# Kernel optimization log

Measured on AMD Instinct MI355X. Metric: run time of the kernel, lower is better.

Reference implementation:

```python
import jax, jax.numpy as jnp
import numpy as np

D = 256; H = 8; DH = D // H; FF = 1024; L = 2048; M = 1024


def _mlp(x, w0, b0, w1, b1, w2, b2):
    # 3-layer MLP, relu on all but last (matches MLP class)
    x = jax.nn.relu(x @ w0 + b0)
    x = jax.nn.relu(x @ w1 + b1)
    return x @ w2 + b2


def _ln(x, g, b, eps=1e-5):
    m = jnp.mean(x, axis=-1, keepdims=True)
    v = jnp.var(x, axis=-1, keepdims=True)
    return (x - m) * jax.lax.rsqrt(v + eps) * g + b


def setup_inputs():
    key = jax.random.key(0)
    ks = jax.random.split(key, 16)
    p = lambda i, shape: jax.random.normal(ks[i], shape, jnp.float32) * 0.02
    z = lambda *s: jnp.zeros(s, jnp.float32)
    o = lambda *s: jnp.ones(s, jnp.float32)
    # positions: ego covers [0, L), agent covers [L-M, 2L-M) -> exactly M shared positions
    return {
        'ego_q': jax.random.normal(ks[0], (1, L, D), jnp.float32),
        'agent_q': jax.random.normal(ks[1], (1, L, D), jnp.float32),
        'ego_pos': jnp.arange(L, dtype=jnp.int32),
        'agent_pos': jnp.arange(L, dtype=jnp.int32) + (L - M),
        'n_match': M,
        'fw0': p(2, (2 * D, D)), 'fb0': z(D),
        'fw1': p(3, (D, D)), 'fb1': z(D),
        'fw2': p(4, (D, D)), 'fb2': z(D),
        'wq': p(5, (D, D)), 'bq': z(D),
        'wk': p(6, (D, D)), 'bk': z(D),
        'wv': p(7, (D, D)), 'bv': z(D),
        'wo': p(8, (D, D)), 'bo': z(D),
        'g1': o(D), 'be1': z(D),
        'l1w': p(9, (D, FF)), 'l1b': z(FF),
        'l2w': p(10, (FF, D)), 'l2b': z(D),
        'g2': o(D), 'be2': z(D),
    }


def reference(ego_q, agent_q, ego_pos, agent_pos, n_match,
              fw0, fb0, fw1, fb1, fw2, fb2,
              wq, bq, wk, bk, wv, bv, wo, bo,
              g1, be1, l1w, l1b, l2w, l2b, g2, be2):
    La = agent_pos.shape[0]
    # vectorized replacement of the per-position dict/loop grouping:
    # for each ego position, find a matching agent position (positions sorted+unique)
    idx = jnp.clip(jnp.searchsorted(agent_pos, ego_pos), 0, La - 1)
    matched = (agent_pos[idx] == ego_pos)                     # (L,)
    pair = jnp.concatenate([ego_q, agent_q[:, idx, :]], axis=-1)  # (1, L, 2D)
    fused = _mlp(pair, fw0, fb0, fw1, fb1, fw2, fb2)          # (1, L, D)
    ego_out = jnp.where(matched[None, :, None], fused, ego_q)
    # agent queries whose positions are NOT in ego's set: indices [n_match, La)
    q = jnp.concatenate([ego_out, agent_q[:, n_match:, :]], axis=1)  # (1, 2L-M, D)
    kv = jnp.concatenate([ego_q, agent_q], axis=1)                   # (1, 2L, D)
    # MultiheadAttention (batch_first, eval mode -> no dropout)
    qh = (q @ wq + bq).reshape(1, -1, H, DH)
    kh = (kv @ wk + bk).reshape(1, -1, H, DH)
    vh = (kv @ wv + bv).reshape(1, -1, H, DH)
    scores = jnp.einsum('bqhd,bkhd->bhqk', qh, kh) * (1.0 / np.sqrt(DH))
    attn = jax.nn.softmax(scores, axis=-1)
    o = jnp.einsum('bhqk,bkhd->bqhd', attn, vh).reshape(1, -1, D) @ wo + bo
    x = _ln(q + o, g1, be1)
    ff = jax.nn.relu(x @ l1w + l1b) @ l2w + l2b
    return _ln(x + ff, g2, be2)
```

## Files before the change

### kernel.cpp

```cpp
#include <hip/hip_runtime.h>
#include <hip/hip_bf16.h>

typedef __hip_bfloat16 bf16;
typedef __bf16 bf16x8 __attribute__((ext_vector_type(8)));
typedef float  f32x16 __attribute__((ext_vector_type(16)));

__device__ __forceinline__ bool is_bf16_flag(const unsigned* g1w) {
    return *g1w == 0x3F803F80u;
}

__device__ __forceinline__ unsigned cvt_pk_bf16(float lo, float hi) {
    unsigned w;
    asm("v_cvt_pk_bf16_f32 %0, %1, %2" : "=v"(w) : "v"(lo), "v"(hi));
    return w;
}
__device__ __forceinline__ void permlane32_swap(unsigned& a, unsigned& b) {
    asm("v_permlane32_swap_b32 %0, %1" : "+v"(a), "+v"(b));
}

union FragU { unsigned u[4]; uint4 q; bf16x8 v; };

__device__ __forceinline__ float loadf(const void* p, size_t i, bool isb) {
    return isb ? __bfloat162float(((const bf16*)p)[i]) : ((const float*)p)[i];
}

__device__ __forceinline__ float4 load4rt(const void* p, size_t i, bool isb) {
    if (isb) {
        uint2 u = *(const uint2*)((const bf16*)p + i);
        float4 f;
        f.x = __uint_as_float(u.x << 16);
        f.y = __uint_as_float(u.x & 0xFFFF0000u);
        f.z = __uint_as_float(u.y << 16);
        f.w = __uint_as_float(u.y & 0xFFFF0000u);
        return f;
    }
    return *(const float4*)((const float*)p + i);
}

__device__ __forceinline__ void store4b(bf16* p, float4 v) {
    uint2 w;
    w.x = cvt_pk_bf16(v.x, v.y);
    w.y = cvt_pk_bf16(v.z, v.w);
    *(uint2*)p = w;
}

__device__ __forceinline__ float4 load4b(const bf16* p) {
    uint2 u = *(const uint2*)p;
    float4 f;
    f.x = __uint_as_float(u.x << 16);
    f.y = __uint_as_float(u.x & 0xFFFF0000u);
    f.z = __uint_as_float(u.y << 16);
    f.w = __uint_as_float(u.y & 0xFFFF0000u);
    return f;
}

#define NCVT 13
#define NWT 9
struct PreArgs {
    const void* csrc[NCVT];
    float*      cdst[NCVT];
    float       cscale[NCVT];
    int         cn4[NCVT];
    int         cblk_end[NCVT];
    int         cvt_blocks;
    const void* wsrc[NWT];
    bf16*       wdst[NWT];
    int         wK[NWT];
    int         wN[NWT];
    float       wscale[NWT];
    int         wblk_end[NWT];
    int         wt_blocks;
    const void* ego; const void* agent;
    const int*  epos; const int* apos;
    int         La;
    bf16*       pair;
    int*        mflag;
};

__global__ void preprocess_kernel(PreArgs a, const unsigned* __restrict__ g1w) {
    bool isb = is_bf16_flag(g1w);
    __shared__ float ld[64][65];
    __shared__ int s_idx[2];
    int b = blockIdx.x;
    int tid = threadIdx.x;
    if (b < a.cvt_blocks) {
        int t = 0;
        while (b >= a.cblk_end[t]) t++;
        int base = (t == 0) ? 0 : a.cblk_end[t - 1];
        int i = (b - base) * 256 + tid;
        if (i >= a.cn4[t]) return;
        float sc = a.cscale[t];
        float4 r = load4rt(a.csrc[t], (size_t)i * 4, isb);
        r.x *= sc; r.y *= sc; r.z *= sc; r.w *= sc;
        ((float4*)a.cdst[t])[i] = r;
    } else if (b < a.cvt_blocks + a.wt_blocks) {
        b -= a.cvt_blocks;
        int w = 0;
        while (b >= a.wblk_end[w]) w++;
        int base = (w == 0) ? 0 : a.wblk_end[w - 1];
        int tt = b - base;
        int tn = a.wN[w] >> 6;
        int kr = (tt / tn) * 64, nc = (tt % tn) * 64;
        int N = a.wN[w], K = a.wK[w];
        float sc = a.wscale[w];
        const void* src = a.wsrc[w];
#pragma unroll
        for (int i = 0; i < 16; i++) {
            int f = tid + i * 256;
            int r = f >> 6, c = f & 63;
            ld[r][c] = loadf(src, (size_t)(kr + r) * N + nc + c, isb) * sc;
        }
        __syncthreads();
        bf16* dst = a.wdst[w];
#pragma unroll
        for (int i = 0; i < 16; i++) {
            int f = tid + i * 256;
            int c = f >> 6, r = f & 63;
            dst[(size_t)(nc + c) * K + kr + r] = __float2bfloat16(ld[r][c]);
        }
    } else {
        b -= a.cvt_blocks + a.wt_blocks;
        int rb = tid >> 7;
        int row = b * 2 + rb;
        int cc = (tid & 127) * 4;
        if ((tid & 127) == 0) {
            int p = a.epos[row];
            int lo = 0, hi = a.La;
            while (lo < hi) { int mid = (lo + hi) >> 1; if (a.apos[mid] < p) lo = mid + 1; else hi = mid; }
            int idx = lo < a.La - 1 ? lo : a.La - 1;
            s_idx[rb] = idx;
            a.mflag[row] = (a.apos[idx] == p) ? 1 : 0;
        }
        __syncthreads();
        int idx = s_idx[rb];
        float4 v = (cc < 256) ? load4rt(a.ego, (size_t)row * 256 + cc, isb)
                              : load4rt(a.agent, (size_t)idx * 256 + (cc - 256), isb);
        store4b(a.pair + (size_t)row * 512 + cc, v);
    }
}

template<int RELU>
__device__ __forceinline__ void gemm_core(const bf16* __restrict__ A, const bf16* __restrict__ Bt,
                                          const float* __restrict__ bias, bf16* __restrict__ C,
                                          int K, int lda, int ldb, int ldc,
                                          int bm, int bn, bool addBias,
                                          char* sA, char* sB) {
    const int t = threadIdx.x;
    const int lane = t & 63, wave = t >> 6;
    const int hi = lane >> 5, ql = lane & 31;
    const int wm = (wave & 1) * 32, wn = (wave >> 1) * 32;

    const int r0 = t >> 3, ch0 = t & 7;
    const int r1 = 32 + r0;
    const int wb0 = (r0 * 128 + ch0 * 16) ^ ((r0 & 7) << 4);
    const int wb1 = (r1 * 128 + ch0 * 16) ^ ((r1 & 7) << 4);

    uint4 ra0, ra1, rb0, rb1;
    {
        ra0 = *(const uint4*)&A [(size_t)(bm + r0) * lda + ch0 * 8];
        ra1 = *(const uint4*)&A [(size_t)(bm + r1) * lda + ch0 * 8];
        rb0 = *(const uint4*)&Bt[(size_t)(bn + r0) * ldb + ch0 * 8];
        rb1 = *(const uint4*)&Bt[(size_t)(bn + r1) * ldb + ch0 * 8];
    }

    f32x16 acc = {};
    const int swzA = ((wm + ql) & 7) << 4;
    const int swzB = ((wn + ql) & 7) << 4;
    const int rowA = (wm + ql) * 128;
    const int rowB = (wn + ql) * 128;

    for (int k0 = 0; k0 < K; k0 += 64) {
        __syncthreads();
        *(uint4*)(sA + wb0) = ra0;
        *(uint4*)(sA + wb1) = ra1;
        *(uint4*)(sB + wb0) = rb0;
        *(uint4*)(sB + wb1) = rb1;
        if (k0 + 64 < K) {
            int kn = k0 + 64;
            ra0 = *(const uint4*)&A [(size_t)(bm + r0) * lda + kn + ch0 * 8];
            ra1 = *(const uint4*)&A [(size_t)(bm + r1) * lda + kn + ch0 * 8];
            rb0 = *(const uint4*)&Bt[(size_t)(bn + r0) * ldb + kn + ch0 * 8];
            rb1 = *(const uint4*)&Bt[(size_t)(bn + r1) * ldb + kn + ch0 * 8];
        }
        __syncthreads();
#pragma unroll
        for (int kc = 0; kc < 4; kc++) {
            FragU af, bf_;
            af.q  = *(const uint4*)(sA + ((rowA + kc * 32 + hi * 16) ^ swzA));
            bf_.q = *(const uint4*)(sB + ((rowB + kc * 32 + hi * 16) ^ swzB));
            acc = __builtin_amdgcn_mfma_f32_32x32x16_bf16(af.v, bf_.v, acc, 0, 0, 0);
        }
    }

    int gn = bn + wn + ql;
    float bsv = addBias ? bias[gn] : 0.f;
#pragma unroll
    for (int r = 0; r < 16; r++) {
        int mrow = (r & 3) + 8 * (r >> 2) + 4 * hi;
        float v = acc[r] + bsv;
        if (RELU) v = fmaxf(v, 0.f);
        C[(size_t)(bm + wm + mrow) * ldc + gn] = __float2bfloat16(v);
    }
}

template<int RELU>
__launch_bounds__(256)
__global__ void gemm_bf16_kernel(const bf16* __restrict__ A, const bf16* __restrict__ Bt,
                                 const float* __restrict__ bias, bf16* __restrict__ C,
                                 int M, int N, int K, int lda, int ldb, int ldc) {
    __shared__ __align__(16) char sA[64 * 128];
    __shared__ __align__(16) char sB[64 * 128];
    const int z = blockIdx.z;
    gemm_core<RELU>(A + (size_t)z * K, Bt + (size_t)z * K, bias, C + (size_t)z * M * ldc,
                    K, lda, ldb, ldc, blockIdx.y * 64, blockIdx.x * 64, z == 0, sA, sB);
}

struct GemmP {
    const bf16* A; const bf16* Bt; const float* bias; bf16* C;
    int K, lda, ldb, ldc, nx;
};

__launch_bounds__(256)
__global__ void gemm_dual_kernel(GemmP p0, GemmP p1, int nblk0) {
    __shared__ __align__(16) char sA[64 * 128];
    __shared__ __align__(16) char sB[64 * 128];
    int b = blockIdx.x;
    const GemmP& p = (b < nblk0) ? p0 : p1;
    int t = (b < nblk0) ? b : b - nblk0;
    int bn = (t % p.nx) * 64, bm = (t / p.nx) * 64;
    gemm_core<0>(p.A, p.Bt, p.bias, p.C, p.K, p.lda, p.ldb, p.ldc, bm, bn, true, sA, sB);
}

__global__ void build_qkv_kernel(const void* __restrict__ ego, const void* __restrict__ agent,
                                 const bf16* __restrict__ fused, const int* __restrict__ mflag,
                                 int L, int Mm, int Nq, int Nk,
                                 bf16* __restrict__ qb, bf16* __restrict__ kvb,
                                 const unsigned* __restrict__ g1w) {
    bool isb = is_bf16_flag(g1w);
    int wave = threadIdx.x >> 6, lane = threadIdx.x & 63;
    int r = blockIdx.x * 4 + wave;
    int col = lane * 4;
    float4 kvv = (r < L) ? load4rt(ego, (size_t)r * 256 + col, isb)
                         : load4rt(agent, (size_t)(r - L) * 256 + col, isb);
    store4b(kvb + (size_t)r * 256 + col, kvv);
    if (r < Nq) {
        float4 qv;
        if (r < L) qv = mflag[r] ? load4b(fused + (size_t)r * 256 + col)
                                 : load4rt(ego, (size_t)r * 256 + col, isb);
        else       qv = load4rt(agent, (size_t)(Mm + r - L) * 256 + col, isb);
        store4b(qb + (size_t)r * 256 + col, qv);
    }
}

#define SPLITS 8

__launch_bounds__(256)
__global__ void attn_mfma_kernel(const bf16* __restrict__ qh,
                                 const bf16* __restrict__ kvh,
                                 float* __restrict__ pm, float* __restrict__ pl,
                                 bf16* __restrict__ pacc,
                                 int Nq, int Nk) {
    __shared__ __align__(16) char sK[64 * 128];
    __shared__ __align__(16) char sV[32 * 128];

    const int h = blockIdx.y, z = blockIdx.z;
    const int t = threadIdx.x;
    const int wave = t >> 6, lane = t & 63;
    const int ql = lane & 31, hi = lane >> 5;
    const int qbase = blockIdx.x * 128 + wave * 32;
    const int kbeg = z * (Nk / SPLITS);
    const int nkk = Nk / SPLITS;

    FragU qf0, qf1;
    {
        const bf16* qp = qh + (size_t)(qbase + ql) * 256 + h * 32;
        qf0.q = *(const uint4*)(qp + hi * 8);
        qf1.q = *(const uint4*)(qp + 16 + hi * 8);
    }

    float mrun = -1e30f, lrun = 0.f;
    f32x16 acc = {};

    const int skey = t >> 2, sch = t & 3;
    const int kwb = (skey * 128 + sch * 16) ^ ((skey & 7) << 4);

    uint4 rk = *(const uint4*)(kvh + (size_t)(kbeg + skey) * 512 + h * 32 + sch * 8);
    uint4 rv = *(const uint4*)(kvh + (size_t)(kbeg + lane) * 512 + 256 + h * 32 + wave * 8);

#pragma unroll 1
    for (int t0 = 0; t0 < nkk; t0 += 64) {
        __syncthreads();
        *(uint4*)(sK + kwb) = rk;
        {
            unsigned short sv[8] = {
                (unsigned short)(rv.x), (unsigned short)(rv.x >> 16),
                (unsigned short)(rv.y), (unsigned short)(rv.y >> 16),
                (unsigned short)(rv.z), (unsigned short)(rv.z >> 16),
                (unsigned short)(rv.w), (unsigned short)(rv.w >> 16)};
#pragma unroll
            for (int i = 0; i < 8; i++) {
                int dh = wave * 8 + i;
                *(unsigned short*)(sV + dh * 128 + ((lane * 2) ^ (i << 4))) = sv[i];
            }
        }
        if (t0 + 64 < nkk) {
            rk = *(const uint4*)(kvh + (size_t)(kbeg + t0 + 64 + skey) * 512 + h * 32 + sch * 8);
            rv = *(const uint4*)(kvh + (size_t)(kbeg + t0 + 64 + lane) * 512 + 256 + h * 32 + wave * 8);
        }
        __syncthreads();

        FragU ka, kb;
        f32x16 s0 = {}, s1 = {};
        {
            int row0 = ql, row1 = 32 + ql;
            int swz = (ql & 7) << 4;
            ka.q = *(const uint4*)(sK + ((row0 * 128 + hi * 16) ^ swz));
            s0 = __builtin_amdgcn_mfma_f32_32x32x16_bf16(ka.v, qf0.v, s0, 0, 0, 0);
            ka.q = *(const uint4*)(sK + ((row0 * 128 + 32 + hi * 16) ^ swz));
            s0 = __builtin_amdgcn_mfma_f32_32x32x16_bf16(ka.v, qf1.v, s0, 0, 0, 0);
            kb.q = *(const uint4*)(sK + ((row1 * 128 + hi * 16) ^ swz));
            s1 = __builtin_amdgcn_mfma_f32_32x32x16_bf16(kb.v, qf0.v, s1, 0, 0, 0);
            kb.q = *(const uint4*)(sK + ((row1 * 128 + 32 + hi * 16) ^ swz));
            s1 = __builtin_amdgcn_mfma_f32_32x32x16_bf16(kb.v, qf1.v, s1, 0, 0, 0);
        }

        float tm = -1e30f;
#pragma unroll
        for (int r = 0; r < 16; r++) tm = fmaxf(tm, fmaxf(s0[r], s1[r]));
        tm = fmaxf(tm, __shfl_xor(tm, 32));
        if (!__all(tm <= mrun)) {
            float mn = fmaxf(mrun, tm);
            float cf = __builtin_amdgcn_exp2f(mrun - mn);
            mrun = mn;
#pragma unroll
            for (int r = 0; r < 16; r++) acc[r] *= cf;
            lrun *= cf;
        }

        float p0[16], p1[16];
        float ls = 0.f;
#pragma unroll
        for (int r = 0; r < 16; r++) { p0[r] = __builtin_amdgcn_exp2f(s0[r] - mrun); ls += p0[r]; }
#pragma unroll
        for (int r = 0; r < 16; r++) { p1[r] = __builtin_amdgcn_exp2f(s1[r] - mrun); ls += p1[r]; }
        ls += __shfl_xor(ls, 32);
        lrun += ls;

        int swz = (ql & 7) << 4;
        FragU vf, pa;
        {
            unsigned a = cvt_pk_bf16(p0[0], p0[1]),  b = cvt_pk_bf16(p0[2], p0[3]);
            unsigned c = cvt_pk_bf16(p0[4], p0[5]),  d = cvt_pk_bf16(p0[6], p0[7]);
            permlane32_swap(a, c); permlane32_swap(b, d);
            pa.u[0] = a; pa.u[1] = b; pa.u[2] = c; pa.u[3] = d;
            vf.q = *(const uint4*)(sV + ((ql * 128 + hi * 16) ^ swz));
            acc = __builtin_amdgcn_mfma_f32_32x32x16_bf16(vf.v, pa.v, acc, 0, 0, 0);
            unsigned e = cvt_pk_bf16(p0[8], p0[9]),   f = cvt_pk_bf16(p0[10], p0[11]);
            unsigned g = cvt_pk_bf16(p0[12], p0[13]), h2 = cvt_pk_bf16(p0[14], p0[15]);
            permlane32_swap(e, g); permlane32_swap(f, h2);
            pa.u[0] = e; pa.u[1] = f; pa.u[2] = g; pa.u[3] = h2;
            vf.q = *(const uint4*)(sV + ((ql * 128 + 32 + hi * 16) ^ swz));
            acc = __builtin_amdgcn_mfma_f32_32x32x16_bf16(vf.v, pa.v, acc, 0, 0, 0);
        }
        {
            unsigned a = cvt_pk_bf16(p1[0], p1[1]),  b = cvt_pk_bf16(p1[2], p1[3]);
            unsigned c = cvt_pk_bf16(p1[4], p1[5]),  d = cvt_pk_bf16(p1[6], p1[7]);
            permlane32_swap(a, c); permlane32_swap(b, d);
            pa.u[0] = a; pa.u[1] = b; pa.u[2] = c; pa.u[3] = d;
            vf.q = *(const uint4*)(sV + ((ql * 128 + 64 + hi * 16) ^ swz));
            acc = __builtin_amdgcn_mfma_f32_32x32x16_bf16(vf.v, pa.v, acc, 0, 0, 0);
            unsigned e = cvt_pk_bf16(p1[8], p1[9]),   f = cvt_pk_bf16(p1[10], p1[11]);
            unsigned g = cvt_pk_bf16(p1[12], p1[13]), h2 = cvt_pk_bf16(p1[14], p1[15]);
            permlane32_swap(e, g); permlane32_swap(f, h2);
            pa.u[0] = e; pa.u[1] = f; pa.u[2] = g; pa.u[3] = h2;
            vf.q = *(const uint4*)(sV + ((ql * 128 + 96 + hi * 16) ^ swz));
            acc = __builtin_amdgcn_mfma_f32_32x32x16_bf16(vf.v, pa.v, acc, 0, 0, 0);
        }
    }

    if (hi == 0) {
        pm[((size_t)z * 8 + h) * Nq + qbase + ql] = mrun;
        pl[((size_t)z * 8 + h) * Nq + qbase + ql] = lrun;
    }
#pragma unroll
    for (int r = 0; r < 16; r++) {
        int dh = (r & 3) + 8 * (r >> 2) + 4 * hi;
        pacc[(((size_t)z * 8 + h) * 32 + dh) * (size_t)Nq + qbase + ql] = __float2bfloat16(acc[r]);
    }
}

__global__ void attn_merge_kernel(const float* __restrict__ pm, const float* __restrict__ pl,
                                  const bf16* __restrict__ pacc, bf16* __restrict__ o, int Nq) {
    int q = blockIdx.x * 256 + threadIdx.x;
    int h = blockIdx.y, dg = blockIdx.z;
    float ml[SPLITS];
    float M = -1e30f;
#pragma unroll
    for (int s = 0; s < SPLITS; s++) {
        ml[s] = pm[((size_t)s * 8 + h) * Nq + q];
        M = fmaxf(M, ml[s]);
    }
    float L = 0.f;
    float w[SPLITS];
#pragma unroll
    for (int s = 0; s < SPLITS; s++) {
        w[s] = __builtin_amdgcn_exp2f(ml[s] - M);
        L += pl[((size_t)s * 8 + h) * Nq + q] * w[s];
    }
    float inv = 1.f / L;
#pragma unroll
    for (int j = 0; j < 4; j++) {
        int d = dg * 4 + j;
        float a = 0.f;
#pragma unroll
        for (int s = 0; s < SPLITS; s++)
            a += __bfloat162float(pacc[(((size_t)s * 8 + h) * 32 + d) * (size_t)Nq + q]) * w[s];
        o[(size_t)q * 256 + h * 32 + d] = __float2bfloat16(a * inv);
    }
}

__global__ void ln_kernel(const bf16* __restrict__ a, const bf16* __restrict__ b,
                          const bf16* __restrict__ c,
                          const float* __restrict__ g, const float* __restrict__ be,
                          bf16* __restrict__ outf16, void* __restrict__ outb,
                          const unsigned* __restrict__ g1w) {
    int wave = threadIdx.x >> 6, lane = threadIdx.x & 63;
    int row = blockIdx.x * 4 + wave;
    int col = lane * 4;
    size_t base = (size_t)row * 256 + col;
    float4 av = load4b(a + base);
    float4 bv = load4b(b + base);
    float x0 = av.x + bv.x, x1 = av.y + bv.y, x2 = av.z + bv.z, x3 = av.w + bv.w;
    if (c) {
        float4 cv = load4b(c + base);
        x0 += cv.x; x1 += cv.y; x2 += cv.z; x3 += cv.w;
    }
    float s  = x0 + x1 + x2 + x3;
    float s2 = x0 * x0 + x1 * x1 + x2 * x2 + x3 * x3;
#pragma unroll
    for (int off = 32; off; off >>= 1) { s += __shfl_xor(s, off); s2 += __shfl_xor(s2, off); }
    float mean = s * (1.f / 256.f);
    float var  = s2 * (1.f / 256.f) - mean * mean;
    float rs = rsqrtf(var + 1e-5f);
    float4 gv = *(const float4*)(g + col);
    float4 bev = *(const float4*)(be + col);
    float y0 = (x0 - mean) * rs * gv.x + bev.x;
    float y1 = (x1 - mean) * rs * gv.y + bev.y;
    float y2 = (x2 - mean) * rs * gv.z + bev.z;
    float y3 = (x3 - mean) * rs * gv.w + bev.w;
    if (outf16) {
        store4b(outf16 + base, make_float4(y0, y1, y2, y3));
    } else if (is_bf16_flag(g1w)) {
        store4b((bf16*)outb + base, make_float4(y0, y1, y2, y3));
    } else {
        *(float4*)((float*)outb + base) = make_float4(y0, y1, y2, y3);
    }
}

extern "C" void kernel_launch(void* const* d_in, const int* in_sizes, int n_in,
                              void* d_out, int out_size, void* d_ws, size_t ws_size,
                              hipStream_t stream) {
    const int Dd = 256;
    const int L  = in_sizes[2];
    const int La = in_sizes[3];
    const int Nk = L + La;
    const int Nq = out_size / Dd;
    const int Mm = L + La - Nq;
    const float scale = 0.17677669529663687f * 1.4426950408889634f;

    const unsigned* g1w = (const unsigned*)d_in[19];

    float* W = (float*)d_ws;
    size_t off = 0;
    auto alloc = [&](size_t n) { size_t o = off; off += n; return o; };
    (void)ws_size; (void)n_in;

    size_t o_fb0 = alloc(256), o_fb1 = alloc(256), o_fb2 = alloc(256);
    size_t o_bq = alloc(256), o_bkv = alloc(512), o_bo = alloc(256);
    size_t o_g1 = alloc(256), o_be1 = alloc(256);
    size_t o_l1b = alloc(1024), o_l2b = alloc(256);
    size_t o_g2 = alloc(256), o_be2 = alloc(256);

    size_t o_fw0t = alloc(65536), o_fw1t = alloc(32768), o_fw2t = alloc(32768);
    size_t o_wqt = alloc(32768), o_wkvt = alloc(65536), o_wot = alloc(32768);
    size_t o_l1wt = alloc(131072), o_l2wt = alloc(131072);
    size_t o_pair = alloc((size_t)L * 256);
    size_t o_h1 = alloc((size_t)L * 128), o_h2 = alloc((size_t)L * 128);
    size_t o_fused = alloc((size_t)L * 128);
    size_t o_q   = alloc((size_t)Nq * 128);
    size_t o_kv  = alloc((size_t)Nk * 128);
    size_t o_qh  = alloc((size_t)Nq * 128);
    size_t o_kvh = alloc((size_t)Nk * 256);
    size_t o_ao  = alloc((size_t)Nq * 128);
    size_t o_opp = alloc((size_t)Nq * 256);
    size_t o_x   = alloc((size_t)Nq * 128);
    size_t o_ff1 = alloc((size_t)Nq * 512);
    size_t o_ff2p = alloc((size_t)Nq * 256);
    size_t o_pacc = alloc((size_t)SPLITS * 8 * 16 * Nq);
    size_t o_pm   = alloc((size_t)SPLITS * 8 * Nq);
    size_t o_pl   = alloc((size_t)SPLITS * 8 * Nq);
    size_t o_ints = alloc((size_t)L);
    int* mflag = (int*)(W + o_ints);

    auto B16 = [&](size_t o) { return (bf16*)(W + o); };

    {
        PreArgs pa;
        const int csrcs[NCVT] = {6, 8, 10, 12, 14, 16, 18, 19, 20, 22, 24, 25, 26};
        const size_t cdsts[NCVT] = {o_fb0, o_fb1, o_fb2, o_bq, o_bkv, o_bkv + 256, o_bo,
                                    o_g1, o_be1, o_l1b, o_l2b, o_g2, o_be2};
        int blk = 0;
        for (int i = 0; i < NCVT; i++) {
            pa.csrc[i] = d_in[csrcs[i]];
            pa.cdst[i] = W + cdsts[i];
            pa.cscale[i] = (csrcs[i] == 12) ? scale : 1.0f;
            pa.cn4[i] = in_sizes[csrcs[i]] / 4;
            blk += (pa.cn4[i] + 255) / 256;
            pa.cblk_end[i] = blk;
        }
        pa.cvt_blocks = blk;

        const int wsrcs[NWT] = {5, 7, 9, 11, 13, 15, 17, 21, 23};
        bf16* wdsts[NWT] = {B16(o_fw0t), B16(o_fw1t), B16(o_fw2t), B16(o_wqt),
                            B16(o_wkvt), B16(o_wkvt) + 65536, B16(o_wot),
                            B16(o_l1wt), B16(o_l2wt)};
        const int Ks[NWT] = {512, 256, 256, 256, 256, 256, 256, 256, 1024};
        const int Ns[NWT] = {256, 256, 256, 256, 256, 256, 256, 1024, 256};
        int wblk = 0;
        for (int i = 0; i < NWT; i++) {
            pa.wsrc[i] = d_in[wsrcs[i]];
            pa.wdst[i] = wdsts[i];
            pa.wK[i] = Ks[i]; pa.wN[i] = Ns[i];
            pa.wscale[i] = (wsrcs[i] == 11) ? scale : 1.0f;
            wblk += (Ks[i] / 64) * (Ns[i] / 64);
            pa.wblk_end[i] = wblk;
        }
        pa.wt_blocks = wblk;

        pa.ego = d_in[0]; pa.agent = d_in[1];
        pa.epos = (const int*)d_in[2]; pa.apos = (const int*)d_in[3];
        pa.La = La; pa.pair = B16(o_pair); pa.mflag = mflag;

        int total = pa.cvt_blocks + pa.wt_blocks + L / 2;
        preprocess_kernel<<<total, 256, 0, stream>>>(pa, g1w);
    }

    gemm_bf16_kernel<1><<<dim3(4, L/64), 256, 0, stream>>>(B16(o_pair), B16(o_fw0t), W + o_fb0, B16(o_h1),    L, 256, 512, 512, 512, 256);
    gemm_bf16_kernel<1><<<dim3(4, L/64), 256, 0, stream>>>(B16(o_h1),   B16(o_fw1t), W + o_fb1, B16(o_h2),    L, 256, 256, 256, 256, 256);
    gemm_bf16_kernel<0><<<dim3(4, L/64), 256, 0, stream>>>(B16(o_h2),   B16(o_fw2t), W + o_fb2, B16(o_fused), L, 256, 256, 256, 256, 256);

    build_qkv_kernel<<<Nk / 4, 256, 0, stream>>>(d_in[0], d_in[1], B16(o_fused), mflag,
                                                 L, Mm, Nq, Nk, B16(o_q), B16(o_kv), g1w);

    {
        GemmP p0{B16(o_q),  B16(o_wqt),  W + o_bq,  B16(o_qh),  256, 256, 256, 256, 4};
        GemmP p1{B16(o_kv), B16(o_wkvt), W + o_bkv, B16(o_kvh), 256, 256, 256, 512, 8};
        int nblk0 = 4 * (Nq / 64);
        int nblk1 = 8 * (Nk / 64);
        gemm_dual_kernel<<<nblk0 + nblk1, 256, 0, stream>>>(p0, p1, nblk0);
    }

    attn_mfma_kernel<<<dim3(Nq/128, 8, SPLITS), 256, 0, stream>>>(B16(o_qh), B16(o_kvh),
                                                                  W + o_pm, W + o_pl, B16(o_pacc),
                                                                  Nq, Nk);
    attn_merge_kernel<<<dim3(Nq/256, 8, 8), 256, 0, stream>>>(W + o_pm, W + o_pl, B16(o_pacc),
                                                              B16(o_ao), Nq);

    gemm_bf16_kernel<0><<<dim3(4, Nq/64, 2), 256, 0, stream>>>(B16(o_ao), B16(o_wot), W + o_bo, B16(o_opp), Nq, 256, 128, 256, 256, 256);
    ln_kernel<<<Nq / 4, 256, 0, stream>>>(B16(o_q), B16(o_opp), B16(o_opp) + (size_t)Nq * 256,
                                          W + o_g1, W + o_be1, B16(o_x), nullptr, g1w);

    gemm_bf16_kernel<1><<<dim3(16, Nq/64), 256, 0, stream>>>(B16(o_x),   B16(o_l1wt), W + o_l1b, B16(o_ff1), Nq, 1024, 256, 256, 256, 1024);
    gemm_bf16_kernel<0><<<dim3(4,  Nq/64, 2), 256, 0, stream>>>(B16(o_ff1), B16(o_l2wt), W + o_l2b, B16(o_ff2p), Nq, 256, 512, 1024, 1024, 256);
    ln_kernel<<<Nq / 4, 256, 0, stream>>>(B16(o_x), B16(o_ff2p), B16(o_ff2p) + (size_t)Nq * 256,
                                          W + o_g2, W + o_be2, nullptr, d_out, g1w);
}
```

Before: 97.48 us.

## Fuse pair/QKV gathers into GEMM A-loads and swizzle attention block order

Removes the materialized pair buffer and the build_qkv kernel by having the GEMMs gather their A rows directly from ego/agent/fused inputs through a loader lambda, converting fp32 to bf16 on the fly. The first LayerNorm also gathers its residual from the sources, so the q/kv staging buffers and one launch go away. The attention kernel gets a flattened, XCD-style swizzled block index and s_setprio around the MFMA sections. In exchange, the GEMM A-loads now do branchy per-row indirection and conversion inside the inner loop.

```diff
diff --git a/kernel.cpp b/kernel.cpp
--- a/kernel.cpp
+++ b/kernel.cpp
@@ -52,6 +52,21 @@
     f.z = __uint_as_float(u.y << 16);
     f.w = __uint_as_float(u.y & 0xFFFF0000u);
     return f;
+}
+
+__device__ __forceinline__ uint4 load8rt(const void* p, size_t off, bool isb) {
+    if (isb) return *(const uint4*)((const bf16*)p + off);
+    const float* f = (const float*)p + off;
+    float4 a = *(const float4*)f, b = *(const float4*)(f + 4);
+    uint4 r;
+    r.x = cvt_pk_bf16(a.x, a.y); r.y = cvt_pk_bf16(a.z, a.w);
+    r.z = cvt_pk_bf16(b.x, b.y); r.w = cvt_pk_bf16(b.z, b.w);
+    return r;
+}
+
+struct RowSrc { const void* p; size_t base; bool b16; };
+__device__ __forceinline__ uint4 load8src(const RowSrc& s, int c) {
+    return load8rt(s.p, s.base + c, s.b16);
 }
 
 #define NCVT 13
@@ -70,17 +85,15 @@
     float       wscale[NWT];
     int         wblk_end[NWT];
     int         wt_blocks;
-    const void* ego; const void* agent;
     const int*  epos; const int* apos;
     int         La;
-    bf16*       pair;
     int*        mflag;
+    int*        midx;
 };
 
 __global__ void preprocess_kernel(PreArgs a, const unsigned* __restrict__ g1w) {
     bool isb = is_bf16_flag(g1w);
     __shared__ float ld[64][65];
-    __shared__ int s_idx[2];
     int b = blockIdx.x;
     int tid = threadIdx.x;
     if (b < a.cvt_blocks) {
@@ -120,29 +133,20 @@
         }
     } else {
         b -= a.cvt_blocks + a.wt_blocks;
-        int rb = tid >> 7;
-        int row = b * 2 + rb;
-        int cc = (tid & 127) * 4;
-        if ((tid & 127) == 0) {
-            int p = a.epos[row];
-            int lo = 0, hi = a.La;
-            while (lo < hi) { int mid = (lo + hi) >> 1; if (a.apos[mid] < p) lo = mid + 1; else hi = mid; }
-            int idx = lo < a.La - 1 ? lo : a.La - 1;
-            s_idx[rb] = idx;
-            a.mflag[row] = (a.apos[idx] == p) ? 1 : 0;
-        }
-        __syncthreads();
-        int idx = s_idx[rb];
-        float4 v = (cc < 256) ? load4rt(a.ego, (size_t)row * 256 + cc, isb)
-                              : load4rt(a.agent, (size_t)idx * 256 + (cc - 256), isb);
-        store4b(a.pair + (size_t)row * 512 + cc, v);
-    }
-}
-
-template<int RELU>
-__device__ __forceinline__ void gemm_core(const bf16* __restrict__ A, const bf16* __restrict__ Bt,
+        int row = b * 256 + tid;
+        int p = a.epos[row];
+        int lo = 0, hi = a.La;
+        while (lo < hi) { int mid = (lo + hi) >> 1; if (a.apos[mid] < p) lo = mid + 1; else hi = mid; }
+        int idx = lo < a.La - 1 ? lo : a.La - 1;
+        a.midx[row] = idx;
+        a.mflag[row] = (a.apos[idx] == p) ? 1 : 0;
+    }
+}
+
+template<int RELU, class AL>
+__device__ __forceinline__ void gemm_core(AL aload, const bf16* __restrict__ Bt,
                                           const float* __restrict__ bias, bf16* __restrict__ C,
-                                          int K, int lda, int ldb, int ldc,
+                                          int K, int ldb, int ldc,
                                           int bm, int bn, bool addBias,
                                           char* sA, char* sB) {
     const int t = threadIdx.x;
@@ -156,12 +160,10 @@
     const int wb1 = (r1 * 128 + ch0 * 16) ^ ((r1 & 7) << 4);
 
     uint4 ra0, ra1, rb0, rb1;
-    {
-        ra0 = *(const uint4*)&A [(size_t)(bm + r0) * lda + ch0 * 8];
-        ra1 = *(const uint4*)&A [(size_t)(bm + r1) * lda + ch0 * 8];
-        rb0 = *(const uint4*)&Bt[(size_t)(bn + r0) * ldb + ch0 * 8];
-        rb1 = *(const uint4*)&Bt[(size_t)(bn + r1) * ldb + ch0 * 8];
-    }
+    ra0 = aload(0, ch0 * 8);
+    ra1 = aload(1, ch0 * 8);
+    rb0 = *(const uint4*)&Bt[(size_t)(bn + r0) * ldb + ch0 * 8];
+    rb1 = *(const uint4*)&Bt[(size_t)(bn + r1) * ldb + ch0 * 8];
 
     f32x16 acc = {};
     const int swzA = ((wm + ql) & 7) << 4;
@@ -177,8 +179,8 @@
         *(uint4*)(sB + wb1) = rb1;
         if (k0 + 64 < K) {
             int kn = k0 + 64;
-            ra0 = *(const uint4*)&A [(size_t)(bm + r0) * lda + kn + ch0 * 8];
-            ra1 = *(const uint4*)&A [(size_t)(bm + r1) * lda + kn + ch0 * 8];
+            ra0 = aload(0, kn + ch0 * 8);
+            ra1 = aload(1, kn + ch0 * 8);
             rb0 = *(const uint4*)&Bt[(size_t)(bn + r0) * ldb + kn + ch0 * 8];
             rb1 = *(const uint4*)&Bt[(size_t)(bn + r1) * ldb + kn + ch0 * 8];
         }
@@ -211,44 +213,79 @@
     __shared__ __align__(16) char sA[64 * 128];
     __shared__ __align__(16) char sB[64 * 128];
     const int z = blockIdx.z;
-    gemm_core<RELU>(A + (size_t)z * K, Bt + (size_t)z * K, bias, C + (size_t)z * M * ldc,
-                    K, lda, ldb, ldc, blockIdx.y * 64, blockIdx.x * 64, z == 0, sA, sB);
-}
-
-struct GemmP {
-    const bf16* A; const bf16* Bt; const float* bias; bf16* C;
-    int K, lda, ldb, ldc, nx;
-};
-
+    const bf16* Az = A + (size_t)z * K;
+    const int bm = blockIdx.y * 64;
+    const int r0 = bm + (threadIdx.x >> 3), r1 = r0 + 32;
+    auto al = [&](int i, int c) {
+        return *(const uint4*)&Az[(size_t)(i ? r1 : r0) * lda + c];
+    };
+    gemm_core<RELU>(al, Bt + (size_t)z * K, bias, C + (size_t)z * M * ldc,
+                    K, ldb, ldc, bm, blockIdx.x * 64, z == 0, sA, sB);
+}
+
+template<int RELU>
 __launch_bounds__(256)
-__global__ void gemm_dual_kernel(GemmP p0, GemmP p1, int nblk0) {
+__global__ void gemm_pair_kernel(const void* __restrict__ ego, const void* __restrict__ agent,
+                                 const int* __restrict__ midx,
+                                 const bf16* __restrict__ Bt, const float* __restrict__ bias,
+                                 bf16* __restrict__ C, int ldc,
+                                 const unsigned* __restrict__ g1w) {
     __shared__ __align__(16) char sA[64 * 128];
     __shared__ __align__(16) char sB[64 * 128];
+    bool isb = is_bf16_flag(g1w);
+    const int bm = blockIdx.y * 64;
+    const int r0 = bm + (threadIdx.x >> 3), r1 = r0 + 32;
+    const int m0 = midx[r0], m1 = midx[r1];
+    auto al = [&](int i, int c) {
+        int r = i ? r1 : r0, m = i ? m1 : m0;
+        if (c < 256) return load8rt(ego, (size_t)r * 256 + c, isb);
+        return load8rt(agent, (size_t)m * 256 + (c - 256), isb);
+    };
+    gemm_core<RELU>(al, Bt, bias, C, 512, 512, ldc, bm, blockIdx.x * 64, true, sA, sB);
+}
+
+__device__ __forceinline__ RowSrc q_row_src(int r, const void* ego, const void* agent,
+                                            const bf16* fused, const int* mflag,
+                                            int L, int Mm, bool isb) {
+    RowSrc s;
+    if (r < L) {
+        if (mflag[r]) { s.p = fused; s.base = (size_t)r * 256; s.b16 = true; }
+        else          { s.p = ego;   s.base = (size_t)r * 256; s.b16 = isb; }
+    } else { s.p = agent; s.base = (size_t)(Mm + r - L) * 256; s.b16 = isb; }
+    return s;
+}
+
+__launch_bounds__(256)
+__global__ void gemm_qkv_kernel(const void* __restrict__ ego, const void* __restrict__ agent,
+                                const bf16* __restrict__ fused, const int* __restrict__ mflag,
+                                int L, int Mm,
+                                const bf16* __restrict__ wqt, const bf16* __restrict__ wkvt,
+                                const float* __restrict__ bq, const float* __restrict__ bkv,
+                                bf16* __restrict__ qh, bf16* __restrict__ kvh, int nblk0,
+                                const unsigned* __restrict__ g1w) {
+    __shared__ __align__(16) char sA[64 * 128];
+    __shared__ __align__(16) char sB[64 * 128];
+    bool isb = is_bf16_flag(g1w);
     int b = blockIdx.x;
-    const GemmP& p = (b < nblk0) ? p0 : p1;
-    int t = (b < nblk0) ? b : b - nblk0;
-    int bn = (t % p.nx) * 64, bm = (t / p.nx) * 64;
-    gemm_core<0>(p.A, p.Bt, p.bias, p.C, p.K, p.lda, p.ldb, p.ldc, bm, bn, true, sA, sB);
-}
-
-__global__ void build_qkv_kernel(const void* __restrict__ ego, const void* __restrict__ agent,
-                                 const bf16* __restrict__ fused, const int* __restrict__ mflag,
-                                 int L, int Mm, int Nq, int Nk,
-                                 bf16* __restrict__ qb, bf16* __restrict__ kvb,
-                                 const unsigned* __restrict__ g1w) {
-    bool isb = is_bf16_flag(g1w);
-    int wave = threadIdx.x >> 6, lane = threadIdx.x & 63;
-    int r = blockIdx.x * 4 + wave;
-    int col = lane * 4;
-    float4 kvv = (r < L) ? load4rt(ego, (size_t)r * 256 + col, isb)
-                         : load4rt(agent, (size_t)(r - L) * 256 + col, isb);
-    store4b(kvb + (size_t)r * 256 + col, kvv);
-    if (r < Nq) {
-        float4 qv;
-        if (r < L) qv = mflag[r] ? load4b(fused + (size_t)r * 256 + col)
-                                 : load4rt(ego, (size_t)r * 256 + col, isb);
-        else       qv = load4rt(agent, (size_t)(Mm + r - L) * 256 + col, isb);
-        store4b(qb + (size_t)r * 256 + col, qv);
+    int rl = threadIdx.x >> 3;
+    if (b < nblk0) {
+        int bn = (b & 3) * 64, bm = (b >> 2) * 64;
+        RowSrc s0 = q_row_src(bm + rl, ego, agent, fused, mflag, L, Mm, isb);
+        RowSrc s1 = q_row_src(bm + rl + 32, ego, agent, fused, mflag, L, Mm, isb);
+        auto al = [&](int i, int c) { return load8src(i ? s1 : s0, c); };
+        gemm_core<0>(al, wqt, bq, qh, 256, 256, 256, bm, bn, true, sA, sB);
+    } else {
+        b -= nblk0;
+        int bn = (b & 7) * 64, bm = (b >> 3) * 64;
+        int r0 = bm + rl, r1 = r0 + 32;
+        RowSrc s0, s1;
+        if (r0 < L) { s0.p = ego; s0.base = (size_t)r0 * 256; }
+        else        { s0.p = agent; s0.base = (size_t)(r0 - L) * 256; }
+        if (r1 < L) { s1.p = ego; s1.base = (size_t)r1 * 256; }
+        else        { s1.p = agent; s1.base = (size_t)(r1 - L) * 256; }
+        s0.b16 = isb; s1.b16 = isb;
+        auto al = [&](int i, int c) { return load8src(i ? s1 : s0, c); };
+        gemm_core<0>(al, wkvt, bkv, kvh, 256, 256, 512, bm, bn, true, sA, sB);
     }
 }
 
@@ -263,11 +300,19 @@
     __shared__ __align__(16) char sK[64 * 128];
     __shared__ __align__(16) char sV[32 * 128];
 
-    const int h = blockIdx.y, z = blockIdx.z;
+    const int nx = Nq >> 7;
+    int bid = blockIdx.x;
+    int per = (nx * 8 * SPLITS) >> 3;
+    int swz = (bid & 7) * per + (bid >> 3);
+    const int x = swz % nx;
+    int rem = swz / nx;
+    const int h = rem & 7;
+    const int z = rem >> 3;
+
     const int t = threadIdx.x;
     const int wave = t >> 6, lane = t & 63;
     const int ql = lane & 31, hi = lane >> 5;
-    const int qbase = blockIdx.x * 128 + wave * 32;
+    const int qbase = x * 128 + wave * 32;
     const int kbeg = z * (Nk / SPLITS);
     const int nkk = Nk / SPLITS;
 
@@ -313,15 +358,17 @@
         f32x16 s0 = {}, s1 = {};
         {
             int row0 = ql, row1 = 32 + ql;
-            int swz = (ql & 7) << 4;
-            ka.q = *(const uint4*)(sK + ((row0 * 128 + hi * 16) ^ swz));
+            int swzk = (ql & 7) << 4;
+            __builtin_amdgcn_s_setprio(1);
+            ka.q = *(const uint4*)(sK + ((row0 * 128 + hi * 16) ^ swzk));
             s0 = __builtin_amdgcn_mfma_f32_32x32x16_bf16(ka.v, qf0.v, s0, 0, 0, 0);
-            ka.q = *(const uint4*)(sK + ((row0 * 128 + 32 + hi * 16) ^ swz));
+            ka.q = *(const uint4*)(sK + ((row0 * 128 + 32 + hi * 16) ^ swzk));
             s0 = __builtin_amdgcn_mfma_f32_32x32x16_bf16(ka.v, qf1.v, s0, 0, 0, 0);
-            kb.q = *(const uint4*)(sK + ((row1 * 128 + hi * 16) ^ swz));
+            kb.q = *(const uint4*)(sK + ((row1 * 128 + hi * 16) ^ swzk));
             s1 = __builtin_amdgcn_mfma_f32_32x32x16_bf16(kb.v, qf0.v, s1, 0, 0, 0);
-            kb.q = *(const uint4*)(sK + ((row1 * 128 + 32 + hi * 16) ^ swz));
+            kb.q = *(const uint4*)(sK + ((row1 * 128 + 32 + hi * 16) ^ swzk));
             s1 = __builtin_amdgcn_mfma_f32_32x32x16_bf16(kb.v, qf1.v, s1, 0, 0, 0);
+            __builtin_amdgcn_s_setprio(0);
         }
 
         float tm = -1e30f;
@@ -346,20 +393,21 @@
         ls += __shfl_xor(ls, 32);
         lrun += ls;
 
-        int swz = (ql & 7) << 4;
+        int swzk = (ql & 7) << 4;
         FragU vf, pa;
+        __builtin_amdgcn_s_setprio(1);
         {
             unsigned a = cvt_pk_bf16(p0[0], p0[1]),  b = cvt_pk_bf16(p0[2], p0[3]);
             unsigned c = cvt_pk_bf16(p0[4], p0[5]),  d = cvt_pk_bf16(p0[6], p0[7]);
             permlane32_swap(a, c); permlane32_swap(b, d);
             pa.u[0] = a; pa.u[1] = b; pa.u[2] = c; pa.u[3] = d;
-            vf.q = *(const uint4*)(sV + ((ql * 128 + hi * 16) ^ swz));
+            vf.q = *(const uint4*)(sV + ((ql * 128 + hi * 16) ^ swzk));
             acc = __builtin_amdgcn_mfma_f32_32x32x16_bf16(vf.v, pa.v, acc, 0, 0, 0);
             unsigned e = cvt_pk_bf16(p0[8], p0[9]),   f = cvt_pk_bf16(p0[10], p0[11]);
             unsigned g = cvt_pk_bf16(p0[12], p0[13]), h2 = cvt_pk_bf16(p0[14], p0[15]);
             permlane32_swap(e, g); permlane32_swap(f, h2);
             pa.u[0] = e; pa.u[1] = f; pa.u[2] = g; pa.u[3] = h2;
-            vf.q = *(const uint4*)(sV + ((ql * 128 + 32 + hi * 16) ^ swz));
+            vf.q = *(const uint4*)(sV + ((ql * 128 + 32 + hi * 16) ^ swzk));
             acc = __builtin_amdgcn_mfma_f32_32x32x16_bf16(vf.v, pa.v, acc, 0, 0, 0);
         }
         {
@@ -367,15 +415,16 @@
             unsigned c = cvt_pk_bf16(p1[4], p1[5]),  d = cvt_pk_bf16(p1[6], p1[7]);
             permlane32_swap(a, c); permlane32_swap(b, d);
             pa.u[0] = a; pa.u[1] = b; pa.u[2] = c; pa.u[3] = d;
-            vf.q = *(const uint4*)(sV + ((ql * 128 + 64 + hi * 16) ^ swz));
+            vf.q = *(const uint4*)(sV + ((ql * 128 + 64 + hi * 16) ^ swzk));
             acc = __builtin_amdgcn_mfma_f32_32x32x16_bf16(vf.v, pa.v, acc, 0, 0, 0);
             unsigned e = cvt_pk_bf16(p1[8], p1[9]),   f = cvt_pk_bf16(p1[10], p1[11]);
             unsigned g = cvt_pk_bf16(p1[12], p1[13]), h2 = cvt_pk_bf16(p1[14], p1[15]);
             permlane32_swap(e, g); permlane32_swap(f, h2);
             pa.u[0] = e; pa.u[1] = f; pa.u[2] = g; pa.u[3] = h2;
-            vf.q = *(const uint4*)(sV + ((ql * 128 + 96 + hi * 16) ^ swz));
+            vf.q = *(const uint4*)(sV + ((ql * 128 + 96 + hi * 16) ^ swzk));
             acc = __builtin_amdgcn_mfma_f32_32x32x16_bf16(vf.v, pa.v, acc, 0, 0, 0);
         }
+        __builtin_amdgcn_s_setprio(0);
     }
 
     if (hi == 0) {
@@ -419,16 +468,28 @@
     }
 }
 
+template<int GATHER>
 __global__ void ln_kernel(const bf16* __restrict__ a, const bf16* __restrict__ b,
                           const bf16* __restrict__ c,
                           const float* __restrict__ g, const float* __restrict__ be,
                           bf16* __restrict__ outf16, void* __restrict__ outb,
+                          const void* __restrict__ ego, const void* __restrict__ agent,
+                          const bf16* __restrict__ fused, const int* __restrict__ mflag,
+                          int L, int Mm,
                           const unsigned* __restrict__ g1w) {
+    bool isb = is_bf16_flag(g1w);
     int wave = threadIdx.x >> 6, lane = threadIdx.x & 63;
     int row = blockIdx.x * 4 + wave;
     int col = lane * 4;
     size_t base = (size_t)row * 256 + col;
-    float4 av = load4b(a + base);
+    float4 av;
+    if (GATHER) {
+        if (row < L) av = mflag[row] ? load4b(fused + base)
+                                     : load4rt(ego, base, isb);
+        else av = load4rt(agent, (size_t)(Mm + row - L) * 256 + col, isb);
+    } else {
+        av = load4b(a + base);
+    }
     float4 bv = load4b(b + base);
     float x0 = av.x + bv.x, x1 = av.y + bv.y, x2 = av.z + bv.z, x3 = av.w + bv.w;
     if (c) {
@@ -484,11 +545,8 @@
     size_t o_fw0t = alloc(65536), o_fw1t = alloc(32768), o_fw2t = alloc(32768);
     size_t o_wqt = alloc(32768), o_wkvt = alloc(65536), o_wot = alloc(32768);
     size_t o_l1wt = alloc(131072), o_l2wt = alloc(131072);
-    size_t o_pair = alloc((size_t)L * 256);
     size_t o_h1 = alloc((size_t)L * 128), o_h2 = alloc((size_t)L * 128);
     size_t o_fused = alloc((size_t)L * 128);
-    size_t o_q   = alloc((size_t)Nq * 128);
-    size_t o_kv  = alloc((size_t)Nk * 128);
     size_t o_qh  = alloc((size_t)Nq * 128);
     size_t o_kvh = alloc((size_t)Nk * 256);
     size_t o_ao  = alloc((size_t)Nq * 128);
@@ -499,8 +557,9 @@
     size_t o_pacc = alloc((size_t)SPLITS * 8 * 16 * Nq);
     size_t o_pm   = alloc((size_t)SPLITS * 8 * Nq);
     size_t o_pl   = alloc((size_t)SPLITS * 8 * Nq);
-    size_t o_ints = alloc((size_t)L);
+    size_t o_ints = alloc((size_t)2 * L);
     int* mflag = (int*)(W + o_ints);
+    int* midx  = mflag + L;
 
     auto B16 = [&](size_t o) { return (bf16*)(W + o); };
 
@@ -537,41 +596,41 @@
         }
         pa.wt_blocks = wblk;
 
-        pa.ego = d_in[0]; pa.agent = d_in[1];
         pa.epos = (const int*)d_in[2]; pa.apos = (const int*)d_in[3];
-        pa.La = La; pa.pair = B16(o_pair); pa.mflag = mflag;
-
-        int total = pa.cvt_blocks + pa.wt_blocks + L / 2;
+        pa.La = La; pa.mflag = mflag; pa.midx = midx;
+
+        int total = pa.cvt_blocks + pa.wt_blocks + L / 256;
         preprocess_kernel<<<total, 256, 0, stream>>>(pa, g1w);
     }
 
-    gemm_bf16_kernel<1><<<dim3(4, L/64), 256, 0, stream>>>(B16(o_pair), B16(o_fw0t), W + o_fb0, B16(o_h1),    L, 256, 512, 512, 512, 256);
-    gemm_bf16_kernel<1><<<dim3(4, L/64), 256, 0, stream>>>(B16(o_h1),   B16(o_fw1t), W + o_fb1, B16(o_h2),    L, 256, 256, 256, 256, 256);
-    gemm_bf16_kernel<0><<<dim3(4, L/64), 256, 0, stream>>>(B16(o_h2),   B16(o_fw2t), W + o_fb2, B16(o_fused), L, 256, 256, 256, 256, 256);
-
-    build_qkv_kernel<<<Nk / 4, 256, 0, stream>>>(d_in[0], d_in[1], B16(o_fused), mflag,
-                                                 L, Mm, Nq, Nk, B16(o_q), B16(o_kv), g1w);
+    gemm_pair_kernel<1><<<dim3(4, L/64), 256, 0, stream>>>(d_in[0], d_in[1], midx,
+                                                           B16(o_fw0t), W + o_fb0, B16(o_h1), 256, g1w);
+    gemm_bf16_kernel<1><<<dim3(4, L/64), 256, 0, stream>>>(B16(o_h1), B16(o_fw1t), W + o_fb1, B16(o_h2),    L, 256, 256, 256, 256, 256);
+    gemm_bf16_kernel<0><<<dim3(4, L/64), 256, 0, stream>>>(B16(o_h2), B16(o_fw2t), W + o_fb2, B16(o_fused), L, 256, 256, 256, 256, 256);
 
     {
-        GemmP p0{B16(o_q),  B16(o_wqt),  W + o_bq,  B16(o_qh),  256, 256, 256, 256, 4};
-        GemmP p1{B16(o_kv), B16(o_wkvt), W + o_bkv, B16(o_kvh), 256, 256, 256, 512, 8};
         int nblk0 = 4 * (Nq / 64);
         int nblk1 = 8 * (Nk / 64);
-        gemm_dual_kernel<<<nblk0 + nblk1, 256, 0, stream>>>(p0, p1, nblk0);
-    }
-
-    attn_mfma_kernel<<<dim3(Nq/128, 8, SPLITS), 256, 0, stream>>>(B16(o_qh), B16(o_kvh),
-                                                                  W + o_pm, W + o_pl, B16(o_pacc),
-                                                                  Nq, Nk);
+        gemm_qkv_kernel<<<nblk0 + nblk1, 256, 0, stream>>>(d_in[0], d_in[1], B16(o_fused), mflag,
+                                                           L, Mm, B16(o_wqt), B16(o_wkvt),
+                                                           W + o_bq, W + o_bkv,
+                                                           B16(o_qh), B16(o_kvh), nblk0, g1w);
+    }
+
+    attn_mfma_kernel<<<(Nq/128) * 8 * SPLITS, 256, 0, stream>>>(B16(o_qh), B16(o_kvh),
+                                                                W + o_pm, W + o_pl, B16(o_pacc),
+                                                                Nq, Nk);
     attn_merge_kernel<<<dim3(Nq/256, 8, 8), 256, 0, stream>>>(W + o_pm, W + o_pl, B16(o_pacc),
                                                               B16(o_ao), Nq);
 
     gemm_bf16_kernel<0><<<dim3(4, Nq/64, 2), 256, 0, stream>>>(B16(o_ao), B16(o_wot), W + o_bo, B16(o_opp), Nq, 256, 128, 256, 256, 256);
-    ln_kernel<<<Nq / 4, 256, 0, stream>>>(B16(o_q), B16(o_opp), B16(o_opp) + (size_t)Nq * 256,
-                                          W + o_g1, W + o_be1, B16(o_x), nullptr, g1w);
+    ln_kernel<1><<<Nq / 4, 256, 0, stream>>>(nullptr, B16(o_opp), B16(o_opp) + (size_t)Nq * 256,
+                                             W + o_g1, W + o_be1, B16(o_x), nullptr,
+                                             d_in[0], d_in[1], B16(o_fused), mflag, L, Mm, g1w);
 
     gemm_bf16_kernel<1><<<dim3(16, Nq/64), 256, 0, stream>>>(B16(o_x),   B16(o_l1wt), W + o_l1b, B16(o_ff1), Nq, 1024, 256, 256, 256, 1024);
     gemm_bf16_kernel<0><<<dim3(4,  Nq/64, 2), 256, 0, stream>>>(B16(o_ff1), B16(o_l2wt), W + o_l2b, B16(o_ff2p), Nq, 256, 512, 1024, 1024, 256);
-    ln_kernel<<<Nq / 4, 256, 0, stream>>>(B16(o_x), B16(o_ff2p), B16(o_ff2p) + (size_t)Nq * 256,
-                                          W + o_g2, W + o_be2, nullptr, d_out, g1w);
-}
+    ln_kernel<0><<<Nq / 4, 256, 0, stream>>>(B16(o_x), B16(o_ff2p), B16(o_ff2p) + (size_t)Nq * 256,
+                                             W + o_g2, W + o_be2, nullptr, d_out,
+                                             nullptr, nullptr, nullptr, nullptr, L, Mm, g1w);
+}
```

Result: slower. 100.2 us (+2.8%).
